# Performance work log

Measured on AMD Instinct MI355X. Metric: run time of the kernel, lower is better.

## Reference

```python
import jax, jax.numpy as jnp
import numpy as np

THRESHOLD = 3.0
MAX_POINTS = 200000


def setup_inputs() -> dict:
    key = jax.random.key(0)
    frames = jax.random.normal(key, (4, 8, 2, 4, 480, 640), dtype=jnp.float32)
    return {"frames": frames}


def reference(frames):
    # frames: [B, S, N_evt, C_evt, H, W]
    B, S, N_evt, C_evt, H, W = frames.shape
    C = N_evt * C_evt
    dense = frames.reshape(B * S, C, H, W)

    # threshold > 0 branch: channel-wise abs-max reduction then threshold
    mask = jnp.max(jnp.abs(dense), axis=1) > THRESHOLD  # [B*S, H, W]

    # jit-compatible compaction: fixed-capacity nonzero (row-major order,
    # deterministic truncation to MAX_POINTS replaces torch's randperm subsample)
    bf, y, x = jnp.nonzero(mask, size=MAX_POINTS, fill_value=0)
    n_valid = jnp.minimum(jnp.sum(mask), MAX_POINTS)
    valid = jnp.arange(MAX_POINTS) < n_valid  # [cap]

    batch_idx = bf // S
    time_idx = bf % S
    coords = jnp.stack((batch_idx, time_idx, y, x), axis=1).astype(jnp.int32)
    coords = jnp.where(valid[:, None], coords, 0)

    features = dense[bf, :, y, x]  # [cap, C] scattered gather
    features = jnp.where(valid[:, None], features, 0.0)

    return features, coords
```

## Files before the change

kernel.cpp:

```cpp
#include <hip/hip_runtime.h>
#include <hip/hip_bf16.h>
#include <stdint.h>

#define HW        307200
#define W_IMG     640
#define TILE      1024
#define NTILES    9600
#define BLK_PER_BF 300
#define MAXPTS    200000
#define COORD_OFF 1600000

#define WS_OFFSETS 65536
#define WS_DATA    131072

__device__ __forceinline__ float comp4(const float4& q, int i) {
    return i == 0 ? q.x : i == 1 ? q.y : i == 2 ? q.z : q.w;
}

__global__ __launch_bounds__(256) void compact_kernel(
        const float* __restrict__ frames, unsigned* __restrict__ counts,
        float* __restrict__ data) {
    __shared__ unsigned s_wsum[4];

    int tid  = threadIdx.x;
    int lane = tid & 63, wave = tid >> 6;
    int tile = blockIdx.x;

    int bf      = tile / BLK_PER_BF;
    int pixBase = (tile - bf * BLK_PER_BF) * TILE + tid * 4;
    const float* base = frames + (size_t)bf * (8 * (size_t)HW) + pixBase;

    float4 v[8];
#pragma unroll
    for (int c = 0; c < 8; ++c)
        v[c] = *(const float4*)(base + (size_t)c * HW);

    float m0 = 0.f, m1 = 0.f, m2 = 0.f, m3 = 0.f;
#pragma unroll
    for (int c = 0; c < 8; ++c) {
        m0 = fmaxf(m0, fabsf(v[c].x));
        m1 = fmaxf(m1, fabsf(v[c].y));
        m2 = fmaxf(m2, fabsf(v[c].z));
        m3 = fmaxf(m3, fabsf(v[c].w));
    }
    int k0 = m0 > 3.0f, k1 = m1 > 3.0f, k2 = m2 > 3.0f, k3 = m3 > 3.0f;
    unsigned cnt = (unsigned)(k0 + k1 + k2 + k3);

    unsigned inc = cnt;
#pragma unroll
    for (int off = 1; off < 64; off <<= 1) {
        unsigned n = __shfl_up(inc, off, 64);
        if (lane >= off) inc += n;
    }
    if (lane == 63) s_wsum[wave] = inc;
    __syncthreads();
    unsigned wbase = 0;
#pragma unroll
    for (int w = 0; w < 4; ++w)
        if (w < wave) wbase += s_wsum[w];
    unsigned excl = wbase + inc - cnt;

    if (tid == 255) counts[tile] = excl + cnt;

    float* tbase = data + (size_t)tile * (TILE * 12);
    unsigned r = excl;
    int k[4] = {k0, k1, k2, k3};
#pragma unroll
    for (int i = 0; i < 4; ++i) {
        if (k[i]) {
            float4* p = (float4*)(tbase + (size_t)r * 12);
            p[0] = make_float4(comp4(v[0], i), comp4(v[1], i),
                               comp4(v[2], i), comp4(v[3], i));
            p[1] = make_float4(comp4(v[4], i), comp4(v[5], i),
                               comp4(v[6], i), comp4(v[7], i));
            int pix = pixBase + i;
            int y = pix / W_IMG;
            int x = pix - y * W_IMG;
            p[2] = make_float4((float)(bf >> 3), (float)(bf & 7),
                               (float)y, (float)x);
            r++;
        }
    }
}

__global__ __launch_bounds__(256) void scan_kernel(const unsigned* __restrict__ counts,
                                                   unsigned* __restrict__ offsets) {
    __shared__ unsigned s[256];
    int tid = threadIdx.x;
    const int per = (NTILES + 255) / 256;
    int begin = tid * per;
    int end   = begin + per > NTILES ? NTILES : begin + per;
    unsigned sum = 0;
    for (int i = begin; i < end; ++i) sum += counts[i];
    s[tid] = sum;
    __syncthreads();
    if (tid == 0) {
        unsigned acc = 0;
        for (int i = 0; i < 256; ++i) { unsigned v = s[i]; s[i] = acc; acc += v; }
    }
    __syncthreads();
    unsigned acc = s[tid];
    for (int i = begin; i < end; ++i) { offsets[i] = acc; acc += counts[i]; }
}

__global__ __launch_bounds__(256) void scatter_kernel(
        const float* __restrict__ data, const unsigned* __restrict__ counts,
        const unsigned* __restrict__ offsets, float* __restrict__ out) {
    int tile = blockIdx.x;
    unsigned g = offsets[tile];
    unsigned c = counts[tile];
    const float* tbase = data + (size_t)tile * (TILE * 12);
    for (unsigned j = threadIdx.x; j < c; j += 256) {
        unsigned r = g + j;
        if (r >= MAXPTS) break;
        const float4* p = (const float4*)(tbase + (size_t)j * 12);
        float4 f0 = p[0], f1 = p[1], co = p[2];
        float4* fo = (float4*)(out + (size_t)r * 8);
        fo[0] = f0;
        fo[1] = f1;
        ((float4*)(out + COORD_OFF))[r] = co;
    }
}

extern "C" void kernel_launch(void* const* d_in, const int* in_sizes, int n_in,
                              void* d_out, int out_size, void* d_ws, size_t ws_size,
                              hipStream_t stream) {
    const float* frames = (const float*)d_in[0];
    float* out = (float*)d_out;

    char* ws = (char*)d_ws;
    unsigned* counts  = (unsigned*)ws;
    unsigned* offsets = (unsigned*)(ws + WS_OFFSETS);
    float*    data    = (float*)(ws + WS_DATA);

    hipMemsetAsync(d_out, 0, (size_t)out_size * sizeof(float), stream);

    compact_kernel<<<NTILES, 256, 0, stream>>>(frames, counts, data);
    scan_kernel<<<1, 256, 0, stream>>>(counts, offsets);
    scatter_kernel<<<NTILES, 256, 0, stream>>>(data, counts, offsets, out);
}
```

Before: 438.0 us.

## Stage compact pixel ids separately and parallelize the tile-offset scan

```diff
diff --git a/kernel.cpp b/kernel.cpp
--- a/kernel.cpp
+++ b/kernel.cpp
@@ -11,7 +11,8 @@
 #define COORD_OFF 1600000
 
 #define WS_OFFSETS 65536
-#define WS_DATA    131072
+#define WS_PIXID   131072
+#define WS_FEATS   39452672
 
 __device__ __forceinline__ float comp4(const float4& q, int i) {
     return i == 0 ? q.x : i == 1 ? q.y : i == 2 ? q.z : q.w;
@@ -19,7 +20,7 @@
 
 __global__ __launch_bounds__(256) void compact_kernel(
         const float* __restrict__ frames, unsigned* __restrict__ counts,
-        float* __restrict__ data) {
+        unsigned* __restrict__ pixid, float* __restrict__ feats) {
     __shared__ unsigned s_wsum[4];
 
     int tid  = threadIdx.x;
@@ -62,63 +63,73 @@
 
     if (tid == 255) counts[tile] = excl + cnt;
 
-    float* tbase = data + (size_t)tile * (TILE * 12);
-    unsigned r = excl;
+    unsigned slot = (unsigned)tile * TILE + excl;
     int k[4] = {k0, k1, k2, k3};
 #pragma unroll
     for (int i = 0; i < 4; ++i) {
         if (k[i]) {
-            float4* p = (float4*)(tbase + (size_t)r * 12);
+            float4* p = (float4*)(feats + (size_t)slot * 8);
             p[0] = make_float4(comp4(v[0], i), comp4(v[1], i),
                                comp4(v[2], i), comp4(v[3], i));
             p[1] = make_float4(comp4(v[4], i), comp4(v[5], i),
                                comp4(v[6], i), comp4(v[7], i));
-            int pix = pixBase + i;
-            int y = pix / W_IMG;
-            int x = pix - y * W_IMG;
-            p[2] = make_float4((float)(bf >> 3), (float)(bf & 7),
-                               (float)y, (float)x);
-            r++;
+            pixid[slot] = (unsigned)bf * HW + (unsigned)(pixBase + i);
+            slot++;
         }
     }
 }
 
 __global__ __launch_bounds__(256) void scan_kernel(const unsigned* __restrict__ counts,
                                                    unsigned* __restrict__ offsets) {
-    __shared__ unsigned s[256];
-    int tid = threadIdx.x;
+    __shared__ unsigned s_w[4];
+    int tid  = threadIdx.x;
+    int lane = tid & 63, wave = tid >> 6;
     const int per = (NTILES + 255) / 256;
     int begin = tid * per;
     int end   = begin + per > NTILES ? NTILES : begin + per;
     unsigned sum = 0;
-    for (int i = begin; i < end; ++i) sum += counts[i];
-    s[tid] = sum;
+    unsigned c[per];
+    for (int i = begin; i < end; ++i) { c[i - begin] = counts[i]; sum += c[i - begin]; }
+
+    unsigned inc = sum;
+#pragma unroll
+    for (int off = 1; off < 64; off <<= 1) {
+        unsigned n = __shfl_up(inc, off, 64);
+        if (lane >= off) inc += n;
+    }
+    if (lane == 63) s_w[wave] = inc;
     __syncthreads();
-    if (tid == 0) {
-        unsigned acc = 0;
-        for (int i = 0; i < 256; ++i) { unsigned v = s[i]; s[i] = acc; acc += v; }
-    }
-    __syncthreads();
-    unsigned acc = s[tid];
-    for (int i = begin; i < end; ++i) { offsets[i] = acc; acc += counts[i]; }
+    unsigned wbase = 0;
+#pragma unroll
+    for (int w = 0; w < 4; ++w)
+        if (w < wave) wbase += s_w[w];
+    unsigned acc = wbase + inc - sum;
+    for (int i = begin; i < end; ++i) { offsets[i] = acc; acc += c[i - begin]; }
 }
 
 __global__ __launch_bounds__(256) void scatter_kernel(
-        const float* __restrict__ data, const unsigned* __restrict__ counts,
-        const unsigned* __restrict__ offsets, float* __restrict__ out) {
+        const float* __restrict__ feats, const unsigned* __restrict__ pixid,
+        const unsigned* __restrict__ counts, const unsigned* __restrict__ offsets,
+        float* __restrict__ out) {
     int tile = blockIdx.x;
     unsigned g = offsets[tile];
     unsigned c = counts[tile];
-    const float* tbase = data + (size_t)tile * (TILE * 12);
     for (unsigned j = threadIdx.x; j < c; j += 256) {
         unsigned r = g + j;
         if (r >= MAXPTS) break;
-        const float4* p = (const float4*)(tbase + (size_t)j * 12);
-        float4 f0 = p[0], f1 = p[1], co = p[2];
+        unsigned slot = (unsigned)tile * TILE + j;
+        const float4* p = (const float4*)(feats + (size_t)slot * 8);
+        float4 f0 = p[0], f1 = p[1];
+        unsigned pid = pixid[slot];
+        unsigned bf  = pid / HW;
+        unsigned pix = pid - bf * HW;
+        unsigned y   = pix / W_IMG;
+        unsigned x   = pix - y * W_IMG;
         float4* fo = (float4*)(out + (size_t)r * 8);
         fo[0] = f0;
         fo[1] = f1;
-        ((float4*)(out + COORD_OFF))[r] = co;
+        ((float4*)(out + COORD_OFF))[r] =
+            make_float4((float)(bf >> 3), (float)(bf & 7), (float)y, (float)x);
     }
 }
 
@@ -131,11 +142,12 @@
     char* ws = (char*)d_ws;
     unsigned* counts  = (unsigned*)ws;
     unsigned* offsets = (unsigned*)(ws + WS_OFFSETS);
-    float*    data    = (float*)(ws + WS_DATA);
+    unsigned* pixid   = (unsigned*)(ws + WS_PIXID);
+    float*    feats   = (float*)(ws + WS_FEATS);
 
     hipMemsetAsync(d_out, 0, (size_t)out_size * sizeof(float), stream);
 
-    compact_kernel<<<NTILES, 256, 0, stream>>>(frames, counts, data);
+    compact_kernel<<<NTILES, 256, 0, stream>>>(frames, counts, pixid, feats);
     scan_kernel<<<1, 256, 0, stream>>>(counts, offsets);
-    scatter_kernel<<<NTILES, 256, 0, stream>>>(data, counts, offsets, out);
+    scatter_kernel<<<NTILES, 256, 0, stream>>>(feats, pixid, counts, offsets, out);
 }
```

Result: no change. 444.9 us (+1.6%).
